# Performance work log

Measured on AMD Instinct MI355X. Metric: run time of the kernel, lower is better.

The kernel has to match this reference:

```python
import jax, jax.numpy as jnp
import numpy as np

IN, OUT, IO, CF, CS = 128, 128, 512, 512, 1024
B = 8192
TAU_IO, TAU_CF, TAU_CS = 2.0, 5.0, 70.0


def _lin(x, W, b):
    # torch nn.Linear: y = x @ W.T + b, W has shape [out, in]
    return x @ W.T + b


def setup_inputs() -> dict:
    key = jax.random.key(0)
    ks = jax.random.split(key, 24)

    def wb(i, fan_out, fan_in):
        s = 1.0 / np.sqrt(fan_in)
        W = jax.random.uniform(ks[2 * i], (fan_out, fan_in), jnp.float32, -s, s)
        b = jax.random.uniform(ks[2 * i + 1], (fan_out,), jnp.float32, -s, s)
        return W, b

    Wi2io, bi2io = wb(0, IO, IN)
    Wio2o, bio2o = wb(1, OUT, IO)
    Wio2io, bio2io = wb(2, IO, IO)
    Wio2cf, bio2cf = wb(3, CF, IO)
    Wcf2io, bcf2io = wb(4, IO, CF)
    Wcf2cs, bcf2cs = wb(5, CS, CF)
    Wcf2cf, bcf2cf = wb(6, CF, CF)
    Wcs2cf, bcs2cf = wb(7, CF, CS)
    Wcs2cs, bcs2cs = wb(8, CS, CS)

    x = jax.random.normal(ks[18], (B, IN), jnp.float32)
    io_state = jnp.zeros((B, IO), jnp.float32)
    cf_state = jnp.zeros((B, CF), jnp.float32)
    cs_state = jnp.zeros((B, CS), jnp.float32)

    return dict(
        x=x, io_state=io_state, cf_state=cf_state, cs_state=cs_state,
        Wi2io=Wi2io, bi2io=bi2io, Wio2o=Wio2o, bio2o=bio2o,
        Wio2io=Wio2io, bio2io=bio2io, Wio2cf=Wio2cf, bio2cf=bio2cf,
        Wcf2io=Wcf2io, bcf2io=bcf2io, Wcf2cs=Wcf2cs, bcf2cs=bcf2cs,
        Wcf2cf=Wcf2cf, bcf2cf=bcf2cf, Wcs2cf=Wcs2cf, bcs2cf=bcs2cf,
        Wcs2cs=Wcs2cs, bcs2cs=bcs2cs,
    )


def reference(x, io_state, cf_state, cs_state,
              Wi2io, bi2io, Wio2o, bio2o,
              Wio2io, bio2io, Wio2cf, bio2cf,
              Wcf2io, bcf2io, Wcf2cs, bcf2cs,
              Wcf2cf, bcf2cf, Wcs2cf, bcs2cf,
              Wcs2cs, bcs2cs):
    x = x.reshape(-1, IN)
    # leaky-integrated updates; all branches read the *previous* states
    io_new = jnp.tanh(
        (1.0 - 1.0 / TAU_IO) * io_state
        + (_lin(io_state, Wio2io, bio2io)
           + _lin(cf_state, Wcf2io, bcf2io)
           + _lin(x, Wi2io, bi2io)) / TAU_IO)
    cf_new = jnp.tanh(
        (1.0 - 1.0 / TAU_CF) * cf_state
        + (_lin(cf_state, Wcf2cf, bcf2cf)
           + _lin(cs_state, Wcs2cf, bcs2cf)
           + _lin(io_state, Wio2cf, bio2cf)) / TAU_CF)
    cs_new = jnp.tanh(
        (1.0 - 1.0 / TAU_CS) * cs_state
        + (_lin(cs_state, Wcs2cs, bcs2cs)
           + _lin(cf_state, Wcf2cs, bcf2cs)) / TAU_CS)
    y = jnp.tanh(_lin(io_new, Wio2o, bio2o))
    return y
```

## Files before the change

### kernel.cpp

```cpp
#include <hip/hip_runtime.h>


typedef float f32x4 __attribute__((ext_vector_type(4)));
typedef __bf16 bf16x4 __attribute__((ext_vector_type(4)));
typedef __bf16 bf16x8 __attribute__((ext_vector_type(8)));
typedef unsigned short u16x4 __attribute__((ext_vector_type(4)));

__device__ __forceinline__ unsigned short f2bf(float f) {
    unsigned u = __builtin_bit_cast(unsigned, f);
    u += 0x7FFFu + ((u >> 16) & 1u);
    return (unsigned short)(u >> 16);
}

__device__ __forceinline__ float tanh_fast(float x) {
    float e = __expf(2.0f * x);
    return 1.0f - 2.0f * __builtin_amdgcn_rcpf(e + 1.0f);
}

__device__ __forceinline__ void gload16(const void* g, void* l) {
    __builtin_amdgcn_global_load_lds(
        (const __attribute__((address_space(1))) void*)g,
        (__attribute__((address_space(3))) void*)l, 16, 0, 0);
}

#define WAITB(N) asm volatile("s_waitcnt vmcnt(" #N ")\n\ts_barrier" ::: "memory")

__global__ __launch_bounds__(256) void k_convert(
    const float* __restrict__ Wi2io, const float* __restrict__ Wio2io,
    const float* __restrict__ Wcf2io, const float* __restrict__ Wio2o,
    const float* __restrict__ b1, const float* __restrict__ b2,
    const float* __restrict__ b3,
    unsigned short* __restrict__ wcat, unsigned short* __restrict__ w2s,
    float* __restrict__ bsum)
{
    int idx = blockIdx.x * 256 + threadIdx.x;
    if (idx < 147456) {
        int n = idx / 288;
        int k = (idx - n * 288) * 4;
        const float* s;
        if (k < 128)      s = Wi2io  + n * 128 + k;
        else if (k < 640) s = Wio2io + n * 512 + (k - 128);
        else              s = Wcf2io + n * 512 + (k - 640);
        f32x4 v = *(const f32x4*)s;
        u16x4 h;
        #pragma unroll
        for (int t = 0; t < 4; ++t) {
            float f = 0.5f * v[t];
            int kk = k + t;
            if (kk >= 128 && kk < 640 && (kk - 128) == n) f += 0.5f;
            h[t] = f2bf(f);
        }
        int ad = n * 1152 + (k & ~63) + ((((k >> 3) & 7) ^ (n & 7)) << 3) + (k & 7);
        *(u16x4*)(wcat + ad) = h;
    } else if (idx < 163840) {
        int q = idx - 147456;
        int n = q >> 7;
        int k = (q & 127) * 4;
        f32x4 v = *(const f32x4*)(Wio2o + n * 512 + k);
        u16x4 h; h[0]=f2bf(v[0]); h[1]=f2bf(v[1]); h[2]=f2bf(v[2]); h[3]=f2bf(v[3]);
        int ad = n * 512 + (k & ~63) + ((((k >> 3) & 7) ^ (n & 7)) << 3) + (k & 7);
        *(u16x4*)(w2s + ad) = h;
    } else if (idx < 164352) {
        int n = idx - 163840;
        bsum[n] = 0.5f * (b1[n] + b2[n] + b3[n]);
    }
}

__global__ __launch_bounds__(512, 2) void k_gemm1(
    const float* __restrict__ x, const float* __restrict__ io,
    const float* __restrict__ cf,
    const unsigned short* __restrict__ wcat,
    const float* __restrict__ bsum,
    unsigned short* __restrict__ ionew)
{
    __shared__ __align__(16) char lds[3][49152];

    const int tid = threadIdx.x, b = blockIdx.x;
    const int xcd = b & 7, idx = b >> 3;
    const int m0 = ((xcd << 3) | (idx & 7)) << 7;
    const int n0 = (idx >> 3) << 7;

    const int lane = tid & 63, wid = tid >> 6;
    const int li = lane & 15, lh = lane >> 4;
    const int wm = (wid >> 1) << 5;
    const int wn = (wid & 1) << 6;

    int a_off_x[4], a_off_s[4], b_off[2];
    #pragma unroll
    for (int j = 0; j < 4; ++j) {
        int r = (wid << 4) + (j << 2) + (lane >> 4);
        int cs = ((lane & 15) ^ (r & 15)) << 2;
        a_off_x[j] = (m0 + r) * 128 + cs;
        a_off_s[j] = (m0 + r) * 512 + cs;
    }
    #pragma unroll
    for (int j = 0; j < 2; ++j) {
        int rb = ((wid << 1) + j) * 8 + (lane >> 3);
        b_off[j] = (n0 + rb) * 1152 + ((lane & 7) << 3);
    }
    const int adstA = wid << 12;
    const int adstB = wid << 11;

    f32x4 zz = {0.f, 0.f, 0.f, 0.f};
    f32x4 acc[2][4];
    #pragma unroll
    for (int i = 0; i < 2; ++i)
        #pragma unroll
        for (int j = 0; j < 4; ++j) acc[i][j] = zz;

#define STAGE1(KT, BUF) do {                                                   \
        int K_ = (KT);                                                         \
        char* A_ = (BUF); char* B_ = (BUF) + 32768;                            \
        if (K_ < 2) {                                                          \
            const float* sp = x + (K_ << 6);                                   \
            _Pragma("unroll")                                                  \
            for (int j = 0; j < 4; ++j)                                        \
                gload16(sp + a_off_x[j], A_ + adstA + (j << 10));              \
        } else if (K_ < 10) {                                                  \
            const float* sp = io + ((K_ - 2) << 6);                            \
            _Pragma("unroll")                                                  \
            for (int j = 0; j < 4; ++j)                                        \
                gload16(sp + a_off_s[j], A_ + adstA + (j << 10));              \
        } else {                                                               \
            const float* sp = cf + ((K_ - 10) << 6);                           \
            _Pragma("unroll")                                                  \
            for (int j = 0; j < 4; ++j)                                        \
                gload16(sp + a_off_s[j], A_ + adstA + (j << 10));              \
        }                                                                      \
        const unsigned short* wp = wcat + (K_ << 6);                           \
        _Pragma("unroll")                                                      \
        for (int j = 0; j < 2; ++j)                                            \
            gload16(wp + b_off[j], B_ + adstB + (j << 10));                    \
    } while (0)

#define COMPUTE1(BUF) do {                                                     \
        const char* A_ = (BUF); const char* B_ = (BUF) + 32768;                \
        _Pragma("unroll")                                                      \
        for (int ks = 0; ks < 2; ++ks) {                                       \
            bf16x8 af[2];                                                      \
            _Pragma("unroll")                                                  \
            for (int mi = 0; mi < 2; ++mi) {                                   \
                int r = wm + mi * 16 + li;                                     \
                int c0 = ks * 8 + lh * 2;                                      \
                f32x4 a0 = *(const f32x4*)(A_ + r * 256 +                      \
                                           ((c0 ^ (r & 15)) << 4));            \
                f32x4 a1 = *(const f32x4*)(A_ + r * 256 +                      \
                                           (((c0 + 1) ^ (r & 15)) << 4));      \
                bf16x4 h0 = __builtin_convertvector(a0, bf16x4);               \
                bf16x4 h1 = __builtin_convertvector(a1, bf16x4);               \
                af[mi] = __builtin_shufflevector(h0, h1, 0,1,2,3,4,5,6,7);     \
            }                                                                  \
            _Pragma("unroll")                                                  \
            for (int nj = 0; nj < 4; ++nj) {                                   \
                int rb = wn + nj * 16 + li;                                    \
                int cb = ks * 4 + lh;                                          \
                bf16x8 bv = *(const bf16x8*)(B_ + rb * 128 +                   \
                                             ((cb ^ (rb & 7)) << 4));          \
                acc[0][nj] = __builtin_amdgcn_mfma_f32_16x16x32_bf16(          \
                    af[0], bv, acc[0][nj], 0, 0, 0);                           \
                acc[1][nj] = __builtin_amdgcn_mfma_f32_16x16x32_bf16(          \
                    af[1], bv, acc[1][nj], 0, 0, 0);                           \
            }                                                                  \
        }                                                                      \
    } while (0)

    STAGE1(0, lds[0]);
    STAGE1(1, lds[1]);
    char* p0 = lds[0]; char* p1 = lds[1]; char* p2 = lds[2];
    #pragma unroll 1
    for (int t = 0; t < 17; ++t) {
        WAITB(6);
        if (t + 2 < 18) STAGE1(t + 2, p2);
        COMPUTE1(p0);
        char* tmp = p0; p0 = p1; p1 = p2; p2 = tmp;
    }
    WAITB(0);
    COMPUTE1(p0);
#undef STAGE1
#undef COMPUTE1

    #pragma unroll
    for (int nj = 0; nj < 4; ++nj) {
        int gn = n0 + wn + nj * 16 + li;
        float bb = bsum[gn];
        #pragma unroll
        for (int mi = 0; mi < 2; ++mi) {
            #pragma unroll
            for (int r = 0; r < 4; ++r) {
                int gm = m0 + wm + mi * 16 + (lh << 2) + r;
                float v = tanh_fast(acc[mi][nj][r] + bb);
                int ad = gm * 512 + (gn & ~63) +
                         ((((gn >> 3) & 7) ^ (gm & 7)) << 3) + (gn & 7);
                ionew[ad] = f2bf(v);
            }
        }
    }
}

__global__ __launch_bounds__(256, 2) void k_gemm2(
    const unsigned short* __restrict__ ionew,
    const unsigned short* __restrict__ w2s,
    const float* __restrict__ b4,
    float* __restrict__ out)
{
    __shared__ __align__(16) char lds[3][20480];

    const int tid = threadIdx.x, b = blockIdx.x;
    const int xcd = b & 7, idx = b >> 3;
    const int m0 = ((xcd << 5) | idx) << 5;

    const int lane = tid & 63, wid = tid >> 6;
    const int li = lane & 15, lh = lane >> 4;
    const int wn = wid << 5;

    const int a2_off = (m0 + (wid << 3) + (lane >> 3)) * 512 + ((lane & 7) << 3);
    int b2_off[4];
    #pragma unroll
    for (int j = 0; j < 4; ++j)
        b2_off[j] = ((wid << 5) + 8 * j + (lane >> 3)) * 512 + ((lane & 7) << 3);

    f32x4 zz = {0.f, 0.f, 0.f, 0.f};
    f32x4 acc[2][2];
    acc[0][0] = zz; acc[0][1] = zz; acc[1][0] = zz; acc[1][1] = zz;

#define STAGE2(KT, BUF) do {                                                   \
        int K_ = (KT);                                                         \
        char* A_ = (BUF); char* B_ = (BUF) + 4096;                             \
        gload16(ionew + a2_off + (K_ << 6), A_ + (wid << 10));                 \
        _Pragma("unroll")                                                      \
        for (int j = 0; j < 4; ++j)                                            \
            gload16(w2s + b2_off[j] + (K_ << 6), B_ + (wid << 12) + j * 1024); \
    } while (0)

#define COMPUTE2(BUF) do {                                                     \
        const char* A_ = (BUF); const char* B_ = (BUF) + 4096;                 \
        _Pragma("unroll")                                                      \
        for (int ks = 0; ks < 2; ++ks) {                                       \
            int c = ks * 4 + lh;                                               \
            bf16x8 av[2];                                                      \
            _Pragma("unroll")                                                  \
            for (int mi = 0; mi < 2; ++mi) {                                   \
                int r = mi * 16 + li;                                          \
                av[mi] = *(const bf16x8*)(A_ + r * 128 + ((c ^ (r & 7)) << 4));\
            }                                                                  \
            _Pragma("unroll")                                                  \
            for (int nj = 0; nj < 2; ++nj) {                                   \
                int rb = wn + nj * 16 + li;                                    \
                bf16x8 bv = *(const bf16x8*)(B_ + rb * 128 +                   \
                                             ((c ^ (rb & 7)) << 4));           \
                acc[0][nj] = __builtin_amdgcn_mfma_f32_16x16x32_bf16(          \
                    av[0], bv, acc[0][nj], 0, 0, 0);                           \
                acc[1][nj] = __builtin_amdgcn_mfma_f32_16x16x32_bf16(          \
                    av[1], bv, acc[1][nj], 0, 0, 0);                           \
            }                                                                  \
        }                                                                      \
    } while (0)

    STAGE2(0, lds[0]);
    STAGE2(1, lds[1]);
    char* p0 = lds[0]; char* p1 = lds[1]; char* p2 = lds[2];
    #pragma unroll 1
    for (int t = 0; t < 7; ++t) {
        WAITB(5);
        if (t + 2 < 8) STAGE2(t + 2, p2);
        COMPUTE2(p0);
        char* tmp = p0; p0 = p1; p1 = p2; p2 = tmp;
    }
    WAITB(0);
    COMPUTE2(p0);
#undef STAGE2
#undef COMPUTE2

    #pragma unroll
    for (int nj = 0; nj < 2; ++nj) {
        int n = wn + nj * 16 + li;
        float bb = b4[n];
        #pragma unroll
        for (int mi = 0; mi < 2; ++mi) {
            #pragma unroll
            for (int r = 0; r < 4; ++r) {
                int gm = m0 + mi * 16 + (lh << 2) + r;
                out[(size_t)gm * 128 + n] = tanh_fast(acc[mi][nj][r] + bb);
            }
        }
    }
}

extern "C" void kernel_launch(void* const* d_in, const int* in_sizes, int n_in,
                              void* d_out, int out_size, void* d_ws, size_t ws_size,
                              hipStream_t stream)
{
    const float* x      = (const float*)d_in[0];
    const float* io     = (const float*)d_in[1];
    const float* cf     = (const float*)d_in[2];
    const float* Wi2io  = (const float*)d_in[4];
    const float* bi2io  = (const float*)d_in[5];
    const float* Wio2o  = (const float*)d_in[6];
    const float* bio2o  = (const float*)d_in[7];
    const float* Wio2io = (const float*)d_in[8];
    const float* bio2io = (const float*)d_in[9];
    const float* Wcf2io = (const float*)d_in[12];
    const float* bcf2io = (const float*)d_in[13];
    float* out = (float*)d_out;

    char* ws = (char*)d_ws;
    unsigned short* wcat  = (unsigned short*)ws;
    unsigned short* w2s   = (unsigned short*)(ws + 1179648);
    float*          bsum  = (float*)(ws + 1310720);
    unsigned short* ionew = (unsigned short*)(ws + 1312768);

    hipLaunchKernelGGL(k_convert, dim3(642), dim3(256), 0, stream,
                       Wi2io, Wio2io, Wcf2io, Wio2o, bi2io, bio2io, bcf2io,
                       wcat, w2s, bsum);
    hipLaunchKernelGGL(k_gemm1, dim3(256), dim3(512), 0, stream,
                       x, io, cf, wcat, bsum, ionew);
    hipLaunchKernelGGL(k_gemm2, dim3(256), dim3(256), 0, stream,
                       ionew, w2s, bio2o, out);
}
```

Baseline: 32.88 us.

## Halve GEMM tile heights to double grid size, use double buffering in gemm1

Splits gemm1 into 64x128 tiles with 256-thread blocks (512 blocks) and changes its triple-buffered pipeline to a double-buffered one with an extra LDS barrier before each refill. Splits gemm2 into 32x64 tiles with 128-thread blocks (512 blocks) by tiling the N dimension. The aim is to fill more CUs on the MI355X (256 blocks underfill 256 CUs with 2 blocks/CU) and cut LDS per block to raise occupancy. The cost is more weight reloads per output and less latency hiding in gemm1's shallower pipeline.

```diff
diff --git a/kernel.cpp b/kernel.cpp
--- a/kernel.cpp
+++ b/kernel.cpp
@@ -24,6 +24,7 @@
 }
 
 #define WAITB(N) asm volatile("s_waitcnt vmcnt(" #N ")\n\ts_barrier" ::: "memory")
+#define BARL()   asm volatile("s_waitcnt lgkmcnt(0)\n\ts_barrier" ::: "memory")
 
 __global__ __launch_bounds__(256) void k_convert(
     const float* __restrict__ Wi2io, const float* __restrict__ Wio2io,
@@ -66,40 +67,36 @@
     }
 }
 
-__global__ __launch_bounds__(512, 2) void k_gemm1(
+__global__ __launch_bounds__(256, 2) void k_gemm1(
     const float* __restrict__ x, const float* __restrict__ io,
     const float* __restrict__ cf,
     const unsigned short* __restrict__ wcat,
     const float* __restrict__ bsum,
     unsigned short* __restrict__ ionew)
 {
-    __shared__ __align__(16) char lds[3][49152];
+    __shared__ __align__(16) char lds[2][32768];
 
     const int tid = threadIdx.x, b = blockIdx.x;
     const int xcd = b & 7, idx = b >> 3;
-    const int m0 = ((xcd << 3) | (idx & 7)) << 7;
-    const int n0 = (idx >> 3) << 7;
+    const int m0 = ((xcd << 4) | (idx & 15)) << 6;
+    const int n0 = (idx >> 4) << 7;
 
     const int lane = tid & 63, wid = tid >> 6;
     const int li = lane & 15, lh = lane >> 4;
     const int wm = (wid >> 1) << 5;
     const int wn = (wid & 1) << 6;
 
-    int a_off_x[4], a_off_s[4], b_off[2];
+    int a_off_x[4], a_off_s[4], b_off[4];
     #pragma unroll
     for (int j = 0; j < 4; ++j) {
         int r = (wid << 4) + (j << 2) + (lane >> 4);
-        int cs = ((lane & 15) ^ (r & 15)) << 2;
-        a_off_x[j] = (m0 + r) * 128 + cs;
-        a_off_s[j] = (m0 + r) * 512 + cs;
-    }
-    #pragma unroll
-    for (int j = 0; j < 2; ++j) {
-        int rb = ((wid << 1) + j) * 8 + (lane >> 3);
+        int cs = (lane & 15) ^ (r & 15);
+        a_off_x[j] = (m0 + r) * 128 + cs * 4;
+        a_off_s[j] = (m0 + r) * 512 + cs * 4;
+        int rb = (wid << 5) + (j << 3) + (lane >> 3);
         b_off[j] = (n0 + rb) * 1152 + ((lane & 7) << 3);
     }
-    const int adstA = wid << 12;
-    const int adstB = wid << 11;
+    const int adst = wid << 12;
 
     f32x4 zz = {0.f, 0.f, 0.f, 0.f};
     f32x4 acc[2][4];
@@ -110,31 +107,31 @@
 
 #define STAGE1(KT, BUF) do {                                                   \
         int K_ = (KT);                                                         \
-        char* A_ = (BUF); char* B_ = (BUF) + 32768;                            \
+        char* A_ = (BUF); char* B_ = (BUF) + 16384;                            \
         if (K_ < 2) {                                                          \
             const float* sp = x + (K_ << 6);                                   \
             _Pragma("unroll")                                                  \
             for (int j = 0; j < 4; ++j)                                        \
-                gload16(sp + a_off_x[j], A_ + adstA + (j << 10));              \
+                gload16(sp + a_off_x[j], A_ + adst + (j << 10));               \
         } else if (K_ < 10) {                                                  \
             const float* sp = io + ((K_ - 2) << 6);                            \
             _Pragma("unroll")                                                  \
             for (int j = 0; j < 4; ++j)                                        \
-                gload16(sp + a_off_s[j], A_ + adstA + (j << 10));              \
+                gload16(sp + a_off_s[j], A_ + adst + (j << 10));               \
         } else {                                                               \
             const float* sp = cf + ((K_ - 10) << 6);                           \
             _Pragma("unroll")                                                  \
             for (int j = 0; j < 4; ++j)                                        \
-                gload16(sp + a_off_s[j], A_ + adstA + (j << 10));              \
+                gload16(sp + a_off_s[j], A_ + adst + (j << 10));               \
         }                                                                      \
         const unsigned short* wp = wcat + (K_ << 6);                           \
         _Pragma("unroll")                                                      \
-        for (int j = 0; j < 2; ++j)                                            \
-            gload16(wp + b_off[j], B_ + adstB + (j << 10));                    \
+        for (int j = 0; j < 4; ++j)                                            \
+            gload16(wp + b_off[j], B_ + adst + (j << 10));                     \
     } while (0)
 
 #define COMPUTE1(BUF) do {                                                     \
-        const char* A_ = (BUF); const char* B_ = (BUF) + 32768;                \
+        const char* A_ = (BUF); const char* B_ = (BUF) + 16384;                \
         _Pragma("unroll")                                                      \
         for (int ks = 0; ks < 2; ++ks) {                                       \
             bf16x8 af[2];                                                      \
@@ -150,12 +147,12 @@
                 bf16x4 h1 = __builtin_convertvector(a1, bf16x4);               \
                 af[mi] = __builtin_shufflevector(h0, h1, 0,1,2,3,4,5,6,7);     \
             }                                                                  \
+            int c = ks * 4 + lh;                                               \
             _Pragma("unroll")                                                  \
             for (int nj = 0; nj < 4; ++nj) {                                   \
                 int rb = wn + nj * 16 + li;                                    \
-                int cb = ks * 4 + lh;                                          \
                 bf16x8 bv = *(const bf16x8*)(B_ + rb * 128 +                   \
-                                             ((cb ^ (rb & 7)) << 4));          \
+                                             ((c ^ (rb & 7)) << 4));           \
                 acc[0][nj] = __builtin_amdgcn_mfma_f32_16x16x32_bf16(          \
                     af[0], bv, acc[0][nj], 0, 0, 0);                           \
                 acc[1][nj] = __builtin_amdgcn_mfma_f32_16x16x32_bf16(          \
@@ -166,16 +163,16 @@
 
     STAGE1(0, lds[0]);
     STAGE1(1, lds[1]);
-    char* p0 = lds[0]; char* p1 = lds[1]; char* p2 = lds[2];
     #pragma unroll 1
-    for (int t = 0; t < 17; ++t) {
-        WAITB(6);
-        if (t + 2 < 18) STAGE1(t + 2, p2);
-        COMPUTE1(p0);
-        char* tmp = p0; p0 = p1; p1 = p2; p2 = tmp;
-    }
-    WAITB(0);
-    COMPUTE1(p0);
+    for (int t = 0; t < 18; ++t) {
+        if (t < 17) { WAITB(8); } else { WAITB(0); }
+        char* cb = lds[t & 1];
+        COMPUTE1(cb);
+        if (t + 2 < 18) {
+            BARL();
+            STAGE1(t + 2, cb);
+        }
+    }
 #undef STAGE1
 #undef COMPUTE1
 
@@ -197,27 +194,33 @@
     }
 }
 
-__global__ __launch_bounds__(256, 2) void k_gemm2(
+__global__ __launch_bounds__(128, 2) void k_gemm2(
     const unsigned short* __restrict__ ionew,
     const unsigned short* __restrict__ w2s,
     const float* __restrict__ b4,
     float* __restrict__ out)
 {
-    __shared__ __align__(16) char lds[3][20480];
+    __shared__ __align__(16) char lds[3][12288];
 
     const int tid = threadIdx.x, b = blockIdx.x;
-    const int xcd = b & 7, idx = b >> 3;
-    const int m0 = ((xcd << 5) | idx) << 5;
+    const int xcd = b & 7, q = b >> 3;
+    const int m0 = ((xcd << 5) | (q & 31)) << 5;
+    const int n0 = (q >> 5) << 6;
 
     const int lane = tid & 63, wid = tid >> 6;
     const int li = lane & 15, lh = lane >> 4;
-    const int wn = wid << 5;
-
-    const int a2_off = (m0 + (wid << 3) + (lane >> 3)) * 512 + ((lane & 7) << 3);
-    int b2_off[4];
-    #pragma unroll
-    for (int j = 0; j < 4; ++j)
-        b2_off[j] = ((wid << 5) + 8 * j + (lane >> 3)) * 512 + ((lane & 7) << 3);
+
+    int a_off[2], b_off[4];
+    #pragma unroll
+    for (int j = 0; j < 2; ++j) {
+        int r = (wid << 4) + (j << 3) + (lane >> 3);
+        a_off[j] = (m0 + r) * 512 + ((lane & 7) << 3);
+    }
+    #pragma unroll
+    for (int j = 0; j < 4; ++j) {
+        int r = (wid << 5) + (j << 3) + (lane >> 3);
+        b_off[j] = (n0 + r) * 512 + ((lane & 7) << 3);
+    }
 
     f32x4 zz = {0.f, 0.f, 0.f, 0.f};
     f32x4 acc[2][2];
@@ -226,10 +229,14 @@
 #define STAGE2(KT, BUF) do {                                                   \
         int K_ = (KT);                                                         \
         char* A_ = (BUF); char* B_ = (BUF) + 4096;                             \
-        gload16(ionew + a2_off + (K_ << 6), A_ + (wid << 10));                 \
+        _Pragma("unroll")                                                      \
+        for (int j = 0; j < 2; ++j)                                            \
+            gload16(ionew + a_off[j] + (K_ << 6),                              \
+                    A_ + (wid << 11) + (j << 10));                             \
         _Pragma("unroll")                                                      \
         for (int j = 0; j < 4; ++j)                                            \
-            gload16(w2s + b2_off[j] + (K_ << 6), B_ + (wid << 12) + j * 1024); \
+            gload16(w2s + b_off[j] + (K_ << 6),                                \
+                    B_ + (wid << 12) + (j << 10));                             \
     } while (0)
 
 #define COMPUTE2(BUF) do {                                                     \
@@ -245,7 +252,7 @@
             }                                                                  \
             _Pragma("unroll")                                                  \
             for (int nj = 0; nj < 2; ++nj) {                                   \
-                int rb = wn + nj * 16 + li;                                    \
+                int rb = (wid << 5) + nj * 16 + li;                            \
                 bf16x8 bv = *(const bf16x8*)(B_ + rb * 128 +                   \
                                              ((c ^ (rb & 7)) << 4));           \
                 acc[0][nj] = __builtin_amdgcn_mfma_f32_16x16x32_bf16(          \
@@ -261,7 +268,7 @@
     char* p0 = lds[0]; char* p1 = lds[1]; char* p2 = lds[2];
     #pragma unroll 1
     for (int t = 0; t < 7; ++t) {
-        WAITB(5);
+        WAITB(6);
         if (t + 2 < 8) STAGE2(t + 2, p2);
         COMPUTE2(p0);
         char* tmp = p0; p0 = p1; p1 = p2; p2 = tmp;
@@ -273,7 +280,7 @@
 
     #pragma unroll
     for (int nj = 0; nj < 2; ++nj) {
-        int n = wn + nj * 16 + li;
+        int n = n0 + (wid << 5) + nj * 16 + li;
         float bb = b4[n];
         #pragma unroll
         for (int mi = 0; mi < 2; ++mi) {
@@ -312,8 +319,8 @@
     hipLaunchKernelGGL(k_convert, dim3(642), dim3(256), 0, stream,
                        Wi2io, Wio2io, Wcf2io, Wio2o, bi2io, bio2io, bcf2io,
                        wcat, w2s, bsum);
-    hipLaunchKernelGGL(k_gemm1, dim3(256), dim3(512), 0, stream,
+    hipLaunchKernelGGL(k_gemm1, dim3(512), dim3(256), 0, stream,
                        x, io, cf, wcat, bsum, ionew);
-    hipLaunchKernelGGL(k_gemm2, dim3(256), dim3(256), 0, stream,
+    hipLaunchKernelGGL(k_gemm2, dim3(512), dim3(128), 0, stream,
                        ionew, w2s, bio2o, out);
 }
```

After: 33.39 us. No clear change (+1.5%).

## Fuse convert and both GEMMs into one persistent kernel with grid barriers

Applied to the files above, without the earlier changes.

Merges the weight-conversion kernel and the two GEMM kernels into a single 256-block kernel, separated by software grid barriers built on global atomics. Phase 2 is re-tiled for 512 threads, with each block covering 32 rows and K staged in 128-wide chunks. The aim is to remove launch gaps between the three kernels. In exchange it adds a memset launch, spin-wait barrier cost, and a deadlock risk if all 256 blocks are not co-resident.

```diff
diff --git a/kernel.cpp b/kernel.cpp
--- a/kernel.cpp
+++ b/kernel.cpp
@@ -24,89 +24,114 @@
 }
 
 #define WAITB(N) asm volatile("s_waitcnt vmcnt(" #N ")\n\ts_barrier" ::: "memory")
-
-__global__ __launch_bounds__(256) void k_convert(
+#define BARL()   asm volatile("s_waitcnt lgkmcnt(0)\n\ts_barrier" ::: "memory")
+
+__device__ __forceinline__ void grid_barrier(unsigned* bar) {
+    __syncthreads();
+    if (threadIdx.x == 0) {
+        __threadfence();
+        unsigned gen = atomicAdd(&bar[1], 0u);
+        __threadfence();
+        unsigned a = atomicAdd(&bar[0], 1u);
+        if (a == 255u) {
+            atomicExch(&bar[0], 0u);
+            __threadfence();
+            atomicAdd(&bar[1], 1u);
+        } else {
+            while (atomicAdd(&bar[1], 0u) == gen)
+                __builtin_amdgcn_s_sleep(16);
+        }
+        __threadfence();
+    }
+    __syncthreads();
+}
+
+__global__ __launch_bounds__(512, 2) void k_all(
+    const float* __restrict__ x, const float* __restrict__ io,
+    const float* __restrict__ cf,
     const float* __restrict__ Wi2io, const float* __restrict__ Wio2io,
     const float* __restrict__ Wcf2io, const float* __restrict__ Wio2o,
     const float* __restrict__ b1, const float* __restrict__ b2,
-    const float* __restrict__ b3,
+    const float* __restrict__ b3, const float* __restrict__ b4,
     unsigned short* __restrict__ wcat, unsigned short* __restrict__ w2s,
-    float* __restrict__ bsum)
+    float* __restrict__ bsum, unsigned short* __restrict__ ionew,
+    unsigned* __restrict__ bar, float* __restrict__ out)
 {
-    int idx = blockIdx.x * 256 + threadIdx.x;
-    if (idx < 147456) {
-        int n = idx / 288;
-        int k = (idx - n * 288) * 4;
-        const float* s;
-        if (k < 128)      s = Wi2io  + n * 128 + k;
-        else if (k < 640) s = Wio2io + n * 512 + (k - 128);
-        else              s = Wcf2io + n * 512 + (k - 640);
-        f32x4 v = *(const f32x4*)s;
-        u16x4 h;
-        #pragma unroll
-        for (int t = 0; t < 4; ++t) {
-            float f = 0.5f * v[t];
-            int kk = k + t;
-            if (kk >= 128 && kk < 640 && (kk - 128) == n) f += 0.5f;
-            h[t] = f2bf(f);
-        }
-        int ad = n * 1152 + (k & ~63) + ((((k >> 3) & 7) ^ (n & 7)) << 3) + (k & 7);
-        *(u16x4*)(wcat + ad) = h;
-    } else if (idx < 163840) {
-        int q = idx - 147456;
-        int n = q >> 7;
-        int k = (q & 127) * 4;
-        f32x4 v = *(const f32x4*)(Wio2o + n * 512 + k);
-        u16x4 h; h[0]=f2bf(v[0]); h[1]=f2bf(v[1]); h[2]=f2bf(v[2]); h[3]=f2bf(v[3]);
-        int ad = n * 512 + (k & ~63) + ((((k >> 3) & 7) ^ (n & 7)) << 3) + (k & 7);
-        *(u16x4*)(w2s + ad) = h;
-    } else if (idx < 164352) {
-        int n = idx - 163840;
-        bsum[n] = 0.5f * (b1[n] + b2[n] + b3[n]);
-    }
-}
-
-__global__ __launch_bounds__(512, 2) void k_gemm1(
-    const float* __restrict__ x, const float* __restrict__ io,
-    const float* __restrict__ cf,
-    const unsigned short* __restrict__ wcat,
-    const float* __restrict__ bsum,
-    unsigned short* __restrict__ ionew)
-{
-    __shared__ __align__(16) char lds[3][49152];
+    __shared__ __align__(16) char lds[147456];
 
     const int tid = threadIdx.x, b = blockIdx.x;
-    const int xcd = b & 7, idx = b >> 3;
-    const int m0 = ((xcd << 3) | (idx & 7)) << 7;
-    const int n0 = (idx >> 3) << 7;
-
     const int lane = tid & 63, wid = tid >> 6;
     const int li = lane & 15, lh = lane >> 4;
-    const int wm = (wid >> 1) << 5;
-    const int wn = (wid & 1) << 6;
-
-    int a_off_x[4], a_off_s[4], b_off[2];
+
     #pragma unroll
-    for (int j = 0; j < 4; ++j) {
-        int r = (wid << 4) + (j << 2) + (lane >> 4);
-        int cs = ((lane & 15) ^ (r & 15)) << 2;
-        a_off_x[j] = (m0 + r) * 128 + cs;
-        a_off_s[j] = (m0 + r) * 512 + cs;
+    for (int it = 0; it < 2; ++it) {
+        int idx = it * 131072 + b * 512 + tid;
+        if (idx < 147456) {
+            int n = idx / 288;
+            int k = (idx - n * 288) * 4;
+            const float* s;
+            if (k < 128)      s = Wi2io  + n * 128 + k;
+            else if (k < 640) s = Wio2io + n * 512 + (k - 128);
+            else              s = Wcf2io + n * 512 + (k - 640);
+            f32x4 v = *(const f32x4*)s;
+            u16x4 h;
+            #pragma unroll
+            for (int t = 0; t < 4; ++t) {
+                float f = 0.5f * v[t];
+                int kk = k + t;
+                if (kk >= 128 && kk < 640 && (kk - 128) == n) f += 0.5f;
+                h[t] = f2bf(f);
+            }
+            int ad = n * 1152 + (k & ~63) +
+                     ((((k >> 3) & 7) ^ (n & 7)) << 3) + (k & 7);
+            *(u16x4*)(wcat + ad) = h;
+        } else if (idx < 163840) {
+            int q = idx - 147456;
+            int n = q >> 7;
+            int k = (q & 127) * 4;
+            f32x4 v = *(const f32x4*)(Wio2o + n * 512 + k);
+            u16x4 h; h[0]=f2bf(v[0]); h[1]=f2bf(v[1]);
+            h[2]=f2bf(v[2]); h[3]=f2bf(v[3]);
+            int ad = n * 512 + (k & ~63) +
+                     ((((k >> 3) & 7) ^ (n & 7)) << 3) + (k & 7);
+            *(u16x4*)(w2s + ad) = h;
+        } else if (idx < 164352) {
+            int n = idx - 163840;
+            bsum[n] = 0.5f * (b1[n] + b2[n] + b3[n]);
+        }
     }
-    #pragma unroll
-    for (int j = 0; j < 2; ++j) {
-        int rb = ((wid << 1) + j) * 8 + (lane >> 3);
-        b_off[j] = (n0 + rb) * 1152 + ((lane & 7) << 3);
-    }
-    const int adstA = wid << 12;
-    const int adstB = wid << 11;
-
-    f32x4 zz = {0.f, 0.f, 0.f, 0.f};
-    f32x4 acc[2][4];
-    #pragma unroll
-    for (int i = 0; i < 2; ++i)
-        #pragma unroll
-        for (int j = 0; j < 4; ++j) acc[i][j] = zz;
+
+    grid_barrier(bar);
+
+    {
+        const int xcd = b & 7, idx1 = b >> 3;
+        const int m0 = ((xcd << 3) | (idx1 & 7)) << 7;
+        const int n0 = (idx1 >> 3) << 7;
+        const int wm = (wid >> 1) << 5;
+        const int wn = (wid & 1) << 6;
+
+        int a_off_x[4], a_off_s[4], b_off[2];
+        #pragma unroll
+        for (int j = 0; j < 4; ++j) {
+            int r = (wid << 4) + (j << 2) + (lane >> 4);
+            int cs = (lane & 15) ^ (r & 15);
+            a_off_x[j] = (m0 + r) * 128 + cs * 4;
+            a_off_s[j] = (m0 + r) * 512 + cs * 4;
+        }
+        #pragma unroll
+        for (int j = 0; j < 2; ++j) {
+            int rb = ((wid << 1) + j) * 8 + (lane >> 3);
+            b_off[j] = (n0 + rb) * 1152 + ((lane & 7) << 3);
+        }
+        const int adstA = wid << 12;
+        const int adstB = wid << 11;
+
+        f32x4 zz = {0.f, 0.f, 0.f, 0.f};
+        f32x4 acc[2][4];
+        #pragma unroll
+        for (int i = 0; i < 2; ++i)
+            #pragma unroll
+            for (int j = 0; j < 4; ++j) acc[i][j] = zz;
 
 #define STAGE1(KT, BUF) do {                                                   \
         int K_ = (KT);                                                         \
@@ -150,12 +175,12 @@
                 bf16x4 h1 = __builtin_convertvector(a1, bf16x4);               \
                 af[mi] = __builtin_shufflevector(h0, h1, 0,1,2,3,4,5,6,7);     \
             }                                                                  \
+            int c = ks * 4 + lh;                                               \
             _Pragma("unroll")                                                  \
             for (int nj = 0; nj < 4; ++nj) {                                   \
                 int rb = wn + nj * 16 + li;                                    \
-                int cb = ks * 4 + lh;                                          \
                 bf16x8 bv = *(const bf16x8*)(B_ + rb * 128 +                   \
-                                             ((cb ^ (rb & 7)) << 4));          \
+                                             ((c ^ (rb & 7)) << 4));           \
                 acc[0][nj] = __builtin_amdgcn_mfma_f32_16x16x32_bf16(          \
                     af[0], bv, acc[0][nj], 0, 0, 0);                           \
                 acc[1][nj] = __builtin_amdgcn_mfma_f32_16x16x32_bf16(          \
@@ -164,123 +189,117 @@
         }                                                                      \
     } while (0)
 
-    STAGE1(0, lds[0]);
-    STAGE1(1, lds[1]);
-    char* p0 = lds[0]; char* p1 = lds[1]; char* p2 = lds[2];
-    #pragma unroll 1
-    for (int t = 0; t < 17; ++t) {
-        WAITB(6);
-        if (t + 2 < 18) STAGE1(t + 2, p2);
+        char* p0 = lds; char* p1 = lds + 49152; char* p2 = lds + 98304;
+        STAGE1(0, p0);
+        STAGE1(1, p1);
+        #pragma unroll 1
+        for (int t = 0; t < 17; ++t) {
+            WAITB(6);
+            if (t + 2 < 18) STAGE1(t + 2, p2);
+            COMPUTE1(p0);
+            char* tmp = p0; p0 = p1; p1 = p2; p2 = tmp;
+        }
+        WAITB(0);
         COMPUTE1(p0);
-        char* tmp = p0; p0 = p1; p1 = p2; p2 = tmp;
-    }
-    WAITB(0);
-    COMPUTE1(p0);
 #undef STAGE1
 #undef COMPUTE1
 
-    #pragma unroll
-    for (int nj = 0; nj < 4; ++nj) {
-        int gn = n0 + wn + nj * 16 + li;
-        float bb = bsum[gn];
-        #pragma unroll
-        for (int mi = 0; mi < 2; ++mi) {
+        #pragma unroll
+        for (int nj = 0; nj < 4; ++nj) {
+            int gn = n0 + wn + nj * 16 + li;
+            float bb = bsum[gn];
             #pragma unroll
-            for (int r = 0; r < 4; ++r) {
-                int gm = m0 + wm + mi * 16 + (lh << 2) + r;
-                float v = tanh_fast(acc[mi][nj][r] + bb);
-                int ad = gm * 512 + (gn & ~63) +
-                         ((((gn >> 3) & 7) ^ (gm & 7)) << 3) + (gn & 7);
-                ionew[ad] = f2bf(v);
+            for (int mi = 0; mi < 2; ++mi) {
+                #pragma unroll
+                for (int r = 0; r < 4; ++r) {
+                    int gm = m0 + wm + mi * 16 + (lh << 2) + r;
+                    float v = tanh_fast(acc[mi][nj][r] + bb);
+                    int ad = gm * 512 + (gn & ~63) +
+                             ((((gn >> 3) & 7) ^ (gm & 7)) << 3) + (gn & 7);
+                    ionew[ad] = f2bf(v);
+                }
             }
         }
     }
-}
-
-__global__ __launch_bounds__(256, 2) void k_gemm2(
-    const unsigned short* __restrict__ ionew,
-    const unsigned short* __restrict__ w2s,
-    const float* __restrict__ b4,
-    float* __restrict__ out)
-{
-    __shared__ __align__(16) char lds[3][20480];
-
-    const int tid = threadIdx.x, b = blockIdx.x;
-    const int xcd = b & 7, idx = b >> 3;
-    const int m0 = ((xcd << 5) | idx) << 5;
-
-    const int lane = tid & 63, wid = tid >> 6;
-    const int li = lane & 15, lh = lane >> 4;
-    const int wn = wid << 5;
-
-    const int a2_off = (m0 + (wid << 3) + (lane >> 3)) * 512 + ((lane & 7) << 3);
-    int b2_off[4];
-    #pragma unroll
-    for (int j = 0; j < 4; ++j)
-        b2_off[j] = ((wid << 5) + 8 * j + (lane >> 3)) * 512 + ((lane & 7) << 3);
-
-    f32x4 zz = {0.f, 0.f, 0.f, 0.f};
-    f32x4 acc[2][2];
-    acc[0][0] = zz; acc[0][1] = zz; acc[1][0] = zz; acc[1][1] = zz;
-
-#define STAGE2(KT, BUF) do {                                                   \
-        int K_ = (KT);                                                         \
-        char* A_ = (BUF); char* B_ = (BUF) + 4096;                             \
-        gload16(ionew + a2_off + (K_ << 6), A_ + (wid << 10));                 \
+
+    grid_barrier(bar);
+
+    {
+        const int m0 = ((((b & 7) << 3) | ((b >> 3) & 7)) << 7) + ((b >> 6) << 5);
+        const int wm = (wid >> 2) << 4;
+        const int wn = (wid & 3) << 5;
+
+        const int arow = (wid >> 1) << 3;
+        const int ahalf = wid & 1;
+        const size_t a_src = (size_t)(m0 + arow + (lane >> 3)) * 512 +
+                             (ahalf << 6) + ((lane & 7) << 3);
+        const int a_dst = (ahalf << 12) + ((wid >> 1) << 10);
+        size_t b_src[4]; int b_dst[4];
+        #pragma unroll
+        for (int j = 0; j < 4; ++j) {
+            int h = j >> 1, rp = j & 1;
+            b_src[j] = (size_t)((wid << 4) + (rp << 3) + (lane >> 3)) * 512 +
+                       (h << 6) + ((lane & 7) << 3);
+            b_dst[j] = (h << 14) + (wid << 11) + (rp << 10);
+        }
+
+        f32x4 zz = {0.f, 0.f, 0.f, 0.f};
+        f32x4 acc2[2];
+        acc2[0] = zz; acc2[1] = zz;
+
+#define P2STAGE(T, BASE) do {                                                  \
+        char* A_ = lds + (BASE); char* B_ = lds + (BASE) + 8192;               \
+        gload16(ionew + a_src + (size_t)(T) * 128, A_ + a_dst);                \
         _Pragma("unroll")                                                      \
         for (int j = 0; j < 4; ++j)                                            \
-            gload16(w2s + b2_off[j] + (K_ << 6), B_ + (wid << 12) + j * 1024); \
+            gload16(w2s + b_src[j] + (size_t)(T) * 128, B_ + b_dst[j]);        \
     } while (0)
 
-#define COMPUTE2(BUF) do {                                                     \
-        const char* A_ = (BUF); const char* B_ = (BUF) + 4096;                 \
+#define P2COMPUTE(BASE) do {                                                   \
+        const char* A_ = lds + (BASE); const char* B_ = lds + (BASE) + 8192;   \
         _Pragma("unroll")                                                      \
-        for (int ks = 0; ks < 2; ++ks) {                                       \
-            int c = ks * 4 + lh;                                               \
-            bf16x8 av[2];                                                      \
-            _Pragma("unroll")                                                  \
-            for (int mi = 0; mi < 2; ++mi) {                                   \
-                int r = mi * 16 + li;                                          \
-                av[mi] = *(const bf16x8*)(A_ + r * 128 + ((c ^ (r & 7)) << 4));\
-            }                                                                  \
+        for (int k4 = 0; k4 < 4; ++k4) {                                       \
+            int h = k4 >> 1;                                                   \
+            int c = (k4 & 1) * 4 + lh;                                         \
+            int r = wm + li;                                                   \
+            bf16x8 af = *(const bf16x8*)(A_ + h * 4096 + r * 128 +             \
+                                         ((c ^ (r & 7)) << 4));                \
             _Pragma("unroll")                                                  \
             for (int nj = 0; nj < 2; ++nj) {                                   \
                 int rb = wn + nj * 16 + li;                                    \
-                bf16x8 bv = *(const bf16x8*)(B_ + rb * 128 +                   \
+                bf16x8 bv = *(const bf16x8*)(B_ + h * 16384 + rb * 128 +       \
                                              ((c ^ (rb & 7)) << 4));           \
-                acc[0][nj] = __builtin_amdgcn_mfma_f32_16x16x32_bf16(          \
-                    av[0], bv, acc[0][nj], 0, 0, 0);                           \
-                acc[1][nj] = __builtin_amdgcn_mfma_f32_16x16x32_bf16(          \
-                    av[1], bv, acc[1][nj], 0, 0, 0);                           \
+                acc2[nj] = __builtin_amdgcn_mfma_f32_16x16x32_bf16(            \
+                    af, bv, acc2[nj], 0, 0, 0);                                \
             }                                                                  \
         }                                                                      \
     } while (0)
 
-    STAGE2(0, lds[0]);
-    STAGE2(1, lds[1]);
-    char* p0 = lds[0]; char* p1 = lds[1]; char* p2 = lds[2];
-    #pragma unroll 1
-    for (int t = 0; t < 7; ++t) {
-        WAITB(5);
-        if (t + 2 < 8) STAGE2(t + 2, p2);
-        COMPUTE2(p0);
-        char* tmp = p0; p0 = p1; p1 = p2; p2 = tmp;
-    }
-    WAITB(0);
-    COMPUTE2(p0);
-#undef STAGE2
-#undef COMPUTE2
-
-    #pragma unroll
-    for (int nj = 0; nj < 2; ++nj) {
-        int n = wn + nj * 16 + li;
-        float bb = b4[n];
-        #pragma unroll
-        for (int mi = 0; mi < 2; ++mi) {
+        P2STAGE(0, 0);
+        P2STAGE(1, 40960);
+        #pragma unroll 1
+        for (int T = 0; T < 4; ++T) {
+            if (T < 3) { WAITB(5); } else { WAITB(0); }
+            int cb = (T & 1) ? 40960 : 0;
+            P2COMPUTE(cb);
+            if (T + 2 < 4) {
+                BARL();
+                P2STAGE(T + 2, cb);
+            }
+        }
+#undef P2STAGE
+#undef P2COMPUTE
+
+        int n = wn + ((lane >> 4) << 0);
+        (void)n;
+        #pragma unroll
+        for (int nj = 0; nj < 2; ++nj) {
+            int col = wn + nj * 16 + li;
+            float bb = b4[col];
             #pragma unroll
             for (int r = 0; r < 4; ++r) {
-                int gm = m0 + mi * 16 + (lh << 2) + r;
-                out[(size_t)gm * 128 + n] = tanh_fast(acc[mi][nj][r] + bb);
+                int row = m0 + wm + (lh << 2) + r;
+                out[(size_t)row * 128 + col] = tanh_fast(acc2[nj][r] + bb);
             }
         }
     }
@@ -308,12 +327,11 @@
     unsigned short* w2s   = (unsigned short*)(ws + 1179648);
     float*          bsum  = (float*)(ws + 1310720);
     unsigned short* ionew = (unsigned short*)(ws + 1312768);
-
-    hipLaunchKernelGGL(k_convert, dim3(642), dim3(256), 0, stream,
-                       Wi2io, Wio2io, Wcf2io, Wio2o, bi2io, bio2io, bcf2io,
-                       wcat, w2s, bsum);
-    hipLaunchKernelGGL(k_gemm1, dim3(256), dim3(512), 0, stream,
-                       x, io, cf, wcat, bsum, ionew);
-    hipLaunchKernelGGL(k_gemm2, dim3(256), dim3(256), 0, stream,
-                       ionew, w2s, bio2o, out);
-}
+    unsigned*       bar   = (unsigned*)(ws + 9701376);
+
+    hipMemsetAsync(bar, 0, 8, stream);
+    hipLaunchKernelGGL(k_all, dim3(256), dim3(512), 0, stream,
+                       x, io, cf, Wi2io, Wio2io, Wcf2io, Wio2o,
+                       bi2io, bio2io, bcf2io, bio2o,
+                       wcat, w2s, bsum, ionew, bar, out);
+}
```

After: 81.20 us. 2.47x slower.
